# Kernel tuning notes

Hardware: AMD Instinct MI355X
Metric: run time of the kernel (lower is better)

The kernel has to match this reference:

```python
import jax, jax.numpy as jnp
import numpy as np


def setup_inputs() -> dict:
    key = jax.random.key(0)
    k1, k2 = jax.random.split(key)
    B, S, V = 8, 512, 30522
    logits = jax.random.normal(k1, (B, S, V), dtype=jnp.float32)
    attention_mask = jax.random.randint(k2, (B, S), 0, 2, dtype=jnp.int32)
    return {"logits": logits, "attention_mask": attention_mask, "top_k": 64}


def reference(logits, attention_mask, top_k):
    # Fused SPLADE activation: log1p(relu(logits)) * mask, max-pooled over seq.
    mask = attention_mask.astype(logits.dtype)[:, :, None]        # (B, S, 1)
    activated = jnp.log1p(jax.nn.relu(logits)) * mask             # (B, S, V)
    values = jnp.max(activated, axis=1)                           # (B, V)
    # Top-k thresholding: zero out everything below the k-th largest value.
    top_values, _ = jax.lax.top_k(values, top_k)                  # (B, k)
    threshold = top_values[..., -1, None]                         # (B, 1)
    return values * (values >= threshold).astype(values.dtype)
```

## Files before the change

kernel.cpp:

```cpp
#include <hip/hip_runtime.h>
#include <hip/hip_bf16.h>

constexpr int B_  = 8;
constexpr int S_  = 512;
constexpr int V_  = 30522;
constexpr int V2_ = V_ / 2;
constexpr int V4_ = V_ / 4;

typedef float f32x4 __attribute__((ext_vector_type(4)));
typedef float f32x2 __attribute__((ext_vector_type(2)));

static __device__ __forceinline__ f32x4 ntload4(const float* p) {
    return __builtin_nontemporal_load(reinterpret_cast<const f32x4*>(p));
}
static __device__ __forceinline__ f32x2 ntload2(const float* p) {
    return __builtin_nontemporal_load(reinterpret_cast<const f32x2*>(p));
}

constexpr int K1_THREADS = 1024;
constexpr int VSPLIT  = 4;
constexpr int SLICE4  = 1908;
constexpr int NS      = 16;
constexpr int NSLOT   = 2;

__global__ __launch_bounds__(K1_THREADS)
void splade_partial_max(const float* __restrict__ logits,
                        const int* __restrict__ mask,
                        float* __restrict__ partial)
{
    __shared__ int s_idx[S_];
    __shared__ int s_cnt;
    const int vs = blockIdx.x;
    const int g  = blockIdx.y;
    const int b  = blockIdx.z;

    if (threadIdx.x < 64) {
        const int lane = threadIdx.x;
        int cnt = 0;
        for (int base = 0; base < S_; base += 64) {
            const int m = mask[b * S_ + base + lane] != 0;
            const unsigned long long bal = __ballot(m);
            if (m) s_idx[cnt + (int)__popcll(bal & ((1ull << lane) - 1ull))] = base + lane;
            cnt += (int)__popcll(bal);
        }
        if (lane == 0) s_cnt = cnt;
    }
    __syncthreads();
    const int n = s_cnt;

    const int len4 = (vs == VSPLIT - 1) ? (V4_ - vs * SLICE4) : SLICE4;
    int  col4[NSLOT];
    bool valid[NSLOT];
#pragma unroll
    for (int p = 0; p < NSLOT; ++p) {
        const int idx4 = threadIdx.x + p * K1_THREADS;
        valid[p] = (idx4 < len4);
        col4[p]  = valid[p] ? (vs * SLICE4 + idx4) : 0;
    }

    f32x4 acc[NSLOT];
#pragma unroll
    for (int p = 0; p < NSLOT; ++p) acc[p] = (f32x4)(0.f);

    const bool do_tail = (vs == VSPLIT - 1) && (threadIdx.x == 0);
    f32x2 acc_t = (f32x2)(0.f);

    int r = g;
    for (; r + NS < n; r += 2 * NS) {
        const int s0 = s_idx[r], s1 = s_idx[r + NS];
        const float* r0 = logits + (size_t)(b * S_ + s0) * V_;
        const float* r1 = logits + (size_t)(b * S_ + s1) * V_;
        f32x4 x0[NSLOT], x1[NSLOT];
#pragma unroll
        for (int p = 0; p < NSLOT; ++p) x0[p] = ntload4(r0 + 4 * col4[p]);
#pragma unroll
        for (int p = 0; p < NSLOT; ++p) x1[p] = ntload4(r1 + 4 * col4[p]);
        if (do_tail) {
            const f32x2 t0 = ntload2(r0 + 2 * (V2_ - 1));
            const f32x2 t1 = ntload2(r1 + 2 * (V2_ - 1));
            acc_t[0] = fmaxf(acc_t[0], fmaxf(t0[0], t1[0]));
            acc_t[1] = fmaxf(acc_t[1], fmaxf(t0[1], t1[1]));
        }
#pragma unroll
        for (int p = 0; p < NSLOT; ++p) {
#pragma unroll
            for (int q = 0; q < 4; ++q)
                acc[p][q] = fmaxf(acc[p][q], fmaxf(x0[p][q], x1[p][q]));
        }
    }
    if (r < n) {
        const float* r0 = logits + (size_t)(b * S_ + s_idx[r]) * V_;
        f32x4 x0[NSLOT];
#pragma unroll
        for (int p = 0; p < NSLOT; ++p) x0[p] = ntload4(r0 + 4 * col4[p]);
        if (do_tail) {
            const f32x2 t0 = ntload2(r0 + 2 * (V2_ - 1));
            acc_t[0] = fmaxf(acc_t[0], t0[0]);
            acc_t[1] = fmaxf(acc_t[1], t0[1]);
        }
#pragma unroll
        for (int p = 0; p < NSLOT; ++p) {
#pragma unroll
            for (int q = 0; q < 4; ++q)
                acc[p][q] = fmaxf(acc[p][q], x0[p][q]);
        }
    }

    float* dst = partial + ((size_t)g * B_ + b) * V_;
#pragma unroll
    for (int p = 0; p < NSLOT; ++p)
        if (valid[p])
            *reinterpret_cast<f32x4*>(dst + 4 * col4[p]) = acc[p];
    if (do_tail)
        *reinterpret_cast<f32x2*>(dst + 2 * (V2_ - 1)) = acc_t;
}

constexpr int KM_THREADS  = 256;
constexpr int KM_BLOCKS_X = (V2_ + KM_THREADS - 1) / KM_THREADS;

__global__ __launch_bounds__(KM_THREADS)
void splade_merge(const float* __restrict__ partial, float* __restrict__ out)
{
    const int b    = blockIdx.y;
    const int idx2 = blockIdx.x * KM_THREADS + threadIdx.x;
    if (idx2 >= V2_) return;
    const float2* p0 = reinterpret_cast<const float2*>(partial) + (size_t)b * V2_ + idx2;
    float2 m = make_float2(0.0f, 0.0f);
#pragma unroll
    for (int gg = 0; gg < NS; ++gg) {
        const float2 x = p0[(size_t)gg * B_ * V2_];
        m.x = fmaxf(m.x, x.x);
        m.y = fmaxf(m.y, x.y);
    }
    reinterpret_cast<float2*>(out)[(size_t)b * V2_ + idx2] = m;
}

constexpr int K2_BLOCK = 1024;
constexpr int NPT2 = (V2_ + K2_BLOCK - 1) / K2_BLOCK;

__global__ __launch_bounds__(K2_BLOCK)
void splade_topk_kernel(float* __restrict__ out,
                        const int* __restrict__ topk_ptr)
{
    const int b = blockIdx.x;
    const int k = topk_ptr[0];
    float2* row2 = reinterpret_cast<float2*>(out) + (size_t)b * V2_;

    unsigned int v[2 * NPT2];
#pragma unroll
    for (int i = 0; i < NPT2; ++i) {
        const int idx2 = threadIdx.x + i * K2_BLOCK;
        float2 x = make_float2(0.0f, 0.0f);
        if (idx2 < V2_) x = row2[idx2];
        v[2 * i]     = __float_as_uint(x.x);
        v[2 * i + 1] = __float_as_uint(x.y);
    }

    __shared__ int s_cnt[32];
    for (int i = threadIdx.x; i < 32; i += K2_BLOCK) s_cnt[i] = 0;
    __syncthreads();

    unsigned int lo = 0u, hi = 0x7f800000u;
    for (int it = 0; it < 32; ++it) {
        if (hi - lo <= 1u) break;
        const unsigned int mid = lo + ((hi - lo) >> 1);
        int c = 0;
#pragma unroll
        for (int i = 0; i < 2 * NPT2; ++i)
            c += (int)__popcll(__ballot(v[i] >= mid));
        if ((threadIdx.x & 63) == 0) atomicAdd(&s_cnt[it], c);
        __syncthreads();
        const int cnt = s_cnt[it];
        if (cnt >= k) lo = mid; else hi = mid;
    }

    const unsigned int T = lo;
#pragma unroll
    for (int i = 0; i < NPT2; ++i) {
        const int idx2 = threadIdx.x + i * K2_BLOCK;
        if (idx2 < V2_) {
            const unsigned int a = v[2 * i], c = v[2 * i + 1];
            float rx = 0.0f, ry = 0.0f;
            if (a >= T) rx = log1pf(__uint_as_float(a));
            if (c >= T) ry = log1pf(__uint_as_float(c));
            row2[idx2] = make_float2(rx, ry);
        }
    }
}

extern "C" void kernel_launch(void* const* d_in, const int* in_sizes, int n_in,
                              void* d_out, int out_size, void* d_ws, size_t ws_size,
                              hipStream_t stream) {
    const float* logits = (const float*)d_in[0];
    const int*   mask   = (const int*)d_in[1];
    const int*   topk   = (const int*)d_in[2];
    float*       out    = (float*)d_out;
    float*       ws     = (float*)d_ws;

    dim3 g1(VSPLIT, NS, B_);
    splade_partial_max<<<g1, K1_THREADS, 0, stream>>>(logits, mask, ws);
    dim3 gm(KM_BLOCKS_X, B_);
    splade_merge<<<gm, KM_THREADS, 0, stream>>>(ws, out);
    splade_topk_kernel<<<B_, K2_BLOCK, 0, stream>>>(out, topk);
}
```

Measured before the change: 90.13 us.

## Replace partial-max workspace and merge kernel with atomicMax into output

The max reduction over sequence now splits the sequence into 8 contiguous chunks instead of 16 interleaved groups. Each block merges its result directly into a zeroed output buffer using unsigned-int atomicMax, which is order-preserving for non-negative floats. This removes the separate merge kernel and the partial workspace round trip, at the cost of a memset, global atomics and fewer blocks (256 vs 512). Nontemporal loads are also replaced with ordinary loads.

Measured after the change: 93.01 us. 1.03x slower.

```diff
diff --git a/kernel.cpp b/kernel.cpp
--- a/kernel.cpp
+++ b/kernel.cpp
@@ -8,42 +8,32 @@
 constexpr int V4_ = V_ / 4;
 
 typedef float f32x4 __attribute__((ext_vector_type(4)));
-typedef float f32x2 __attribute__((ext_vector_type(2)));
-
-static __device__ __forceinline__ f32x4 ntload4(const float* p) {
-    return __builtin_nontemporal_load(reinterpret_cast<const f32x4*>(p));
-}
-static __device__ __forceinline__ f32x2 ntload2(const float* p) {
-    return __builtin_nontemporal_load(reinterpret_cast<const f32x2*>(p));
-}
 
 constexpr int K1_THREADS = 1024;
 constexpr int VSPLIT  = 4;
 constexpr int SLICE4  = 1908;
-constexpr int NS      = 16;
+constexpr int NSCHUNK = 8;
+constexpr int SCHUNK  = S_ / NSCHUNK;
 constexpr int NSLOT   = 2;
 
 __global__ __launch_bounds__(K1_THREADS)
-void splade_partial_max(const float* __restrict__ logits,
-                        const int* __restrict__ mask,
-                        float* __restrict__ partial)
+void splade_max_atomic(const float* __restrict__ logits,
+                       const int* __restrict__ mask,
+                       unsigned int* __restrict__ out_bits)
 {
-    __shared__ int s_idx[S_];
+    __shared__ int s_idx[SCHUNK];
     __shared__ int s_cnt;
     const int vs = blockIdx.x;
-    const int g  = blockIdx.y;
+    const int sc = blockIdx.y;
     const int b  = blockIdx.z;
+    const int s0 = sc * SCHUNK;
 
     if (threadIdx.x < 64) {
         const int lane = threadIdx.x;
-        int cnt = 0;
-        for (int base = 0; base < S_; base += 64) {
-            const int m = mask[b * S_ + base + lane] != 0;
-            const unsigned long long bal = __ballot(m);
-            if (m) s_idx[cnt + (int)__popcll(bal & ((1ull << lane) - 1ull))] = base + lane;
-            cnt += (int)__popcll(bal);
-        }
-        if (lane == 0) s_cnt = cnt;
+        const int m = mask[b * S_ + s0 + lane] != 0;
+        const unsigned long long bal = __ballot(m);
+        if (m) s_idx[(int)__popcll(bal & ((1ull << lane) - 1ull))] = lane;
+        if (lane == 0) s_cnt = (int)__popcll(bal);
     }
     __syncthreads();
     const int n = s_cnt;
@@ -63,23 +53,25 @@
     for (int p = 0; p < NSLOT; ++p) acc[p] = (f32x4)(0.f);
 
     const bool do_tail = (vs == VSPLIT - 1) && (threadIdx.x == 0);
-    f32x2 acc_t = (f32x2)(0.f);
+    float tail0 = 0.f, tail1 = 0.f;
 
-    int r = g;
-    for (; r + NS < n; r += 2 * NS) {
-        const int s0 = s_idx[r], s1 = s_idx[r + NS];
-        const float* r0 = logits + (size_t)(b * S_ + s0) * V_;
-        const float* r1 = logits + (size_t)(b * S_ + s1) * V_;
+    int r = 0;
+    for (; r + 1 < n; r += 2) {
+        const int s0i = s_idx[r], s1i = s_idx[r + 1];
+        const float* r0 = logits + (size_t)(b * S_ + s0 + s0i) * V_;
+        const float* r1 = logits + (size_t)(b * S_ + s0 + s1i) * V_;
         f32x4 x0[NSLOT], x1[NSLOT];
 #pragma unroll
-        for (int p = 0; p < NSLOT; ++p) x0[p] = ntload4(r0 + 4 * col4[p]);
+        for (int p = 0; p < NSLOT; ++p)
+            x0[p] = *reinterpret_cast<const f32x4*>(r0 + 4 * col4[p]);
 #pragma unroll
-        for (int p = 0; p < NSLOT; ++p) x1[p] = ntload4(r1 + 4 * col4[p]);
+        for (int p = 0; p < NSLOT; ++p)
+            x1[p] = *reinterpret_cast<const f32x4*>(r1 + 4 * col4[p]);
         if (do_tail) {
-            const f32x2 t0 = ntload2(r0 + 2 * (V2_ - 1));
-            const f32x2 t1 = ntload2(r1 + 2 * (V2_ - 1));
-            acc_t[0] = fmaxf(acc_t[0], fmaxf(t0[0], t1[0]));
-            acc_t[1] = fmaxf(acc_t[1], fmaxf(t0[1], t1[1]));
+            const float2 t0 = *reinterpret_cast<const float2*>(r0 + 2 * (V2_ - 1));
+            const float2 t1 = *reinterpret_cast<const float2*>(r1 + 2 * (V2_ - 1));
+            tail0 = fmaxf(tail0, fmaxf(t0.x, t1.x));
+            tail1 = fmaxf(tail1, fmaxf(t0.y, t1.y));
         }
 #pragma unroll
         for (int p = 0; p < NSLOT; ++p) {
@@ -89,14 +81,15 @@
         }
     }
     if (r < n) {
-        const float* r0 = logits + (size_t)(b * S_ + s_idx[r]) * V_;
+        const float* r0 = logits + (size_t)(b * S_ + s0 + s_idx[r]) * V_;
         f32x4 x0[NSLOT];
 #pragma unroll
-        for (int p = 0; p < NSLOT; ++p) x0[p] = ntload4(r0 + 4 * col4[p]);
+        for (int p = 0; p < NSLOT; ++p)
+            x0[p] = *reinterpret_cast<const f32x4*>(r0 + 4 * col4[p]);
         if (do_tail) {
-            const f32x2 t0 = ntload2(r0 + 2 * (V2_ - 1));
-            acc_t[0] = fmaxf(acc_t[0], t0[0]);
-            acc_t[1] = fmaxf(acc_t[1], t0[1]);
+            const float2 t0 = *reinterpret_cast<const float2*>(r0 + 2 * (V2_ - 1));
+            tail0 = fmaxf(tail0, t0.x);
+            tail1 = fmaxf(tail1, t0.y);
         }
 #pragma unroll
         for (int p = 0; p < NSLOT; ++p) {
@@ -106,54 +99,40 @@
         }
     }
 
-    float* dst = partial + ((size_t)g * B_ + b) * V_;
+    unsigned int* o = out_bits + (size_t)b * V_;
 #pragma unroll
-    for (int p = 0; p < NSLOT; ++p)
-        if (valid[p])
-            *reinterpret_cast<f32x4*>(dst + 4 * col4[p]) = acc[p];
-    if (do_tail)
-        *reinterpret_cast<f32x2*>(dst + 2 * (V2_ - 1)) = acc_t;
-}
-
-constexpr int KM_THREADS  = 256;
-constexpr int KM_BLOCKS_X = (V2_ + KM_THREADS - 1) / KM_THREADS;
-
-__global__ __launch_bounds__(KM_THREADS)
-void splade_merge(const float* __restrict__ partial, float* __restrict__ out)
-{
-    const int b    = blockIdx.y;
-    const int idx2 = blockIdx.x * KM_THREADS + threadIdx.x;
-    if (idx2 >= V2_) return;
-    const float2* p0 = reinterpret_cast<const float2*>(partial) + (size_t)b * V2_ + idx2;
-    float2 m = make_float2(0.0f, 0.0f);
+    for (int p = 0; p < NSLOT; ++p) {
+        if (valid[p]) {
 #pragma unroll
-    for (int gg = 0; gg < NS; ++gg) {
-        const float2 x = p0[(size_t)gg * B_ * V2_];
-        m.x = fmaxf(m.x, x.x);
-        m.y = fmaxf(m.y, x.y);
+            for (int q = 0; q < 4; ++q)
+                atomicMax(o + 4 * col4[p] + q, __float_as_uint(acc[p][q]));
+        }
     }
-    reinterpret_cast<float2*>(out)[(size_t)b * V2_ + idx2] = m;
+    if (do_tail) {
+        atomicMax(o + 2 * (V2_ - 1),     __float_as_uint(tail0));
+        atomicMax(o + 2 * (V2_ - 1) + 1, __float_as_uint(tail1));
+    }
 }
 
 constexpr int K2_BLOCK = 1024;
 constexpr int NPT2 = (V2_ + K2_BLOCK - 1) / K2_BLOCK;
 
 __global__ __launch_bounds__(K2_BLOCK)
-void splade_topk_kernel(float* __restrict__ out,
+void splade_topk_kernel(unsigned int* __restrict__ out_bits,
                         const int* __restrict__ topk_ptr)
 {
     const int b = blockIdx.x;
     const int k = topk_ptr[0];
-    float2* row2 = reinterpret_cast<float2*>(out) + (size_t)b * V2_;
+    uint2* row2 = reinterpret_cast<uint2*>(out_bits) + (size_t)b * V2_;
 
     unsigned int v[2 * NPT2];
 #pragma unroll
     for (int i = 0; i < NPT2; ++i) {
         const int idx2 = threadIdx.x + i * K2_BLOCK;
-        float2 x = make_float2(0.0f, 0.0f);
+        uint2 x = make_uint2(0u, 0u);
         if (idx2 < V2_) x = row2[idx2];
-        v[2 * i]     = __float_as_uint(x.x);
-        v[2 * i + 1] = __float_as_uint(x.y);
+        v[2 * i]     = x.x;
+        v[2 * i + 1] = x.y;
     }
 
     __shared__ int s_cnt[32];
@@ -175,6 +154,7 @@
     }
 
     const unsigned int T = lo;
+    float2* frow2 = reinterpret_cast<float2*>(row2);
 #pragma unroll
     for (int i = 0; i < NPT2; ++i) {
         const int idx2 = threadIdx.x + i * K2_BLOCK;
@@ -183,7 +163,7 @@
             float rx = 0.0f, ry = 0.0f;
             if (a >= T) rx = log1pf(__uint_as_float(a));
             if (c >= T) ry = log1pf(__uint_as_float(c));
-            row2[idx2] = make_float2(rx, ry);
+            frow2[idx2] = make_float2(rx, ry);
         }
     }
 }
@@ -194,12 +174,11 @@
     const float* logits = (const float*)d_in[0];
     const int*   mask   = (const int*)d_in[1];
     const int*   topk   = (const int*)d_in[2];
-    float*       out    = (float*)d_out;
-    float*       ws     = (float*)d_ws;
+    unsigned int* out   = (unsigned int*)d_out;
 
-    dim3 g1(VSPLIT, NS, B_);
-    splade_partial_max<<<g1, K1_THREADS, 0, stream>>>(logits, mask, ws);
-    dim3 gm(KM_BLOCKS_X, B_);
-    splade_merge<<<gm, KM_THREADS, 0, stream>>>(ws, out);
+    hipMemsetAsync(out, 0, (size_t)out_size * sizeof(float), stream);
+
+    dim3 g1(VSPLIT, NSCHUNK, B_);
+    splade_max_atomic<<<g1, K1_THREADS, 0, stream>>>(logits, mask, out);
     splade_topk_kernel<<<B_, K2_BLOCK, 0, stream>>>(out, topk);
 }
```
